# Performance work log

Hardware: AMD Instinct MI355X
Metric: run time of the kernel (lower is better)

The kernel has to match this reference:

```python
import jax, jax.numpy as jnp
import numpy as np

N_NODES = 100000


def setup_inputs() -> dict:
    key = jax.random.key(0)
    k1, k2, k3, k4, k5, k6 = jax.random.split(key, 6)
    n_edges = 1600000
    X = jax.random.normal(k1, (N_NODES, 256), dtype=jnp.float32)
    edge_row = jax.random.randint(k2, (n_edges,), 0, N_NODES, dtype=jnp.int64)
    edge_col = jax.random.randint(k3, (n_edges,), 0, N_NODES, dtype=jnp.int64)
    edge_val = jax.random.uniform(k4, (n_edges,), dtype=jnp.float32)
    W = jax.random.normal(k5, (128, 256), dtype=jnp.float32) * 0.05
    b = jax.random.normal(k6, (128,), dtype=jnp.float32) * 0.05
    return {"X": X, "edge_row": edge_row, "edge_col": edge_col,
            "edge_val": edge_val, "W": W, "b": b}


def reference(X, edge_row, edge_col, edge_val, W, b):
    # Dense projection: H = X @ W^T + b  -> [N, out_dim]
    H = jnp.einsum('ni,oi->no', X, W) + b
    # SpMM: out[r] = sum_e A[r, c_e] * H[c_e] over edges with row r
    msgs = edge_val[:, None] * H[edge_col]          # [E, out_dim]
    out = jax.ops.segment_sum(msgs, edge_row, num_segments=N_NODES)
    return out
```

## Files before the change

### kernel.cpp

```cpp
#include <hip/hip_runtime.h>
#include <hip/hip_bf16.h>

#define NNODES 100000
#define NEDGES 1600000
#define KDIM 256
#define ODIM 128
#define NXCD 8
#define NB_SCAN 391
#define EDGE_CAP 1900032
#define ESTRIDE 400000
#define GEMM_BLOCKS 1563
#define RANK_BLOCKS 1563

typedef __attribute__((ext_vector_type(8))) short short8;
typedef __attribute__((ext_vector_type(4))) float floatx4;

static __device__ __forceinline__ short f2bf(float f) {
  union { float f; unsigned u; } x; x.f = f;
  unsigned r = (x.u + 0x7fffu + ((x.u >> 16) & 1u)) >> 16;
  return (short)r;
}

__global__ void conv_w_kernel(const float* __restrict__ W, short* __restrict__ Wb) {
  int i = blockIdx.x * 256 + threadIdx.x;
  if (i < ODIM * KDIM) Wb[i] = f2bf(W[i]);
}

__global__ void scan1_kernel(const unsigned* __restrict__ counts, int* __restrict__ chunkExcl,
                             int* __restrict__ blockSums) {
  __shared__ int s[256];
  int t = threadIdx.x;
  int n = blockIdx.x * 256 + t;
  int sum = 0;
  if (n < NNODES) {
    int s0 = 0;
#pragma unroll
    for (int x = 0; x < NXCD; x++) s0 += (int)counts[(size_t)x * NNODES + n];
    sum = (s0 + 3) & ~3;
  }
  s[t] = sum;
  __syncthreads();
  for (int o = 1; o < 256; o <<= 1) {
    int add = (t >= o) ? s[t - o] : 0;
    __syncthreads();
    s[t] += add;
    __syncthreads();
  }
  if (n < NNODES) chunkExcl[n] = s[t] - sum;
  if (t == 255) blockSums[blockIdx.x] = s[255];
}

__global__ void scan2_kernel(const int* __restrict__ blockSums, int* __restrict__ blockBase,
                             int* __restrict__ offsets) {
  __shared__ int s[512];
  int t = threadIdx.x;
  int v = (t < NB_SCAN) ? blockSums[t] : 0;
  s[t] = v;
  __syncthreads();
  for (int o = 1; o < 512; o <<= 1) {
    int add = (t >= o) ? s[t - o] : 0;
    __syncthreads();
    s[t] += add;
    __syncthreads();
  }
  if (t < NB_SCAN) blockBase[t] = s[t] - v;
  if (t == 511) offsets[NNODES] = s[511];
}

__global__ void scan3_kernel(const int* __restrict__ chunkExcl, const int* __restrict__ blockBase,
                             unsigned* __restrict__ counts, int* __restrict__ offsets) {
  int n = blockIdx.x * 256 + threadIdx.x;
  if (n >= NNODES) return;
  int run = chunkExcl[n] + blockBase[n >> 8];
  offsets[n] = run;
#pragma unroll
  for (int x = 0; x < NXCD; x++) {
    int c = (int)counts[(size_t)x * NNODES + n];
    counts[(size_t)x * NNODES + n] = (unsigned)run;
    run += c;
  }
}

__global__ void place_kernel(const int* __restrict__ rows, const int* __restrict__ cols,
                             const float* __restrict__ vals,
                             const unsigned short* __restrict__ rank,
                             const unsigned* __restrict__ sbase, int2* __restrict__ edges) {
  int i = blockIdx.x * 256 + threadIdx.x;
#pragma unroll
  for (int j = 0; j < 4; j++) {
    int e = i + j * ESTRIDE;
    if (e < NEDGES) {
      int r = rows[e];
      unsigned rk = rank[e];
      int p = (int)sbase[(size_t)(rk >> 8) * NNODES + r] + (int)(rk & 255u);
      int2 rec;
      rec.x = cols[e];
      rec.y = __float_as_int(vals[e]);
      edges[p] = rec;
    }
  }
}

__global__ __launch_bounds__(256) void gemm_rank_kernel(
    const float* __restrict__ X, const short* __restrict__ Wb,
    const float* __restrict__ bias, unsigned* __restrict__ H2,
    const int* __restrict__ rows, unsigned* __restrict__ counts,
    unsigned short* __restrict__ rank) {
  if (blockIdx.x < RANK_BLOCKS) {
    unsigned xcc;
    asm("s_getreg_b32 %0, hwreg(HW_REG_XCC_ID)" : "=s"(xcc));
    xcc &= 7u;
    unsigned* cbase = counts + (size_t)xcc * NNODES;
    int i = blockIdx.x * 256 + threadIdx.x;
#pragma unroll
    for (int j = 0; j < 4; j++) {
      int e = i + j * ESTRIDE;
      if (e < NEDGES) {
        int r = rows[e];
        unsigned old = __hip_atomic_fetch_add(&cbase[r], 1u, __ATOMIC_RELAXED,
                                              __HIP_MEMORY_SCOPE_WORKGROUP);
        rank[e] = (unsigned short)((xcc << 8) | old);
      }
    }
    return;
  }
  const int gb = blockIdx.x - RANK_BLOCKS;
  const int lane = threadIdx.x & 63;
  const int wave = threadIdx.x >> 6;
  const int l16 = lane & 15;
  const int quad = lane >> 4;
  const int rowBase = gb * 64 + wave * 16;
  const int arow = rowBase + l16;
  const bool inb = arow < NNODES;
  const float4 zf4 = {0.f, 0.f, 0.f, 0.f};
  const float4* xp = (const float4*)(X + (size_t)(inb ? arow : 0) * KDIM + quad * 8);

  floatx4 acc[8];
#pragma unroll
  for (int t = 0; t < 8; t++) acc[t] = (floatx4){0.f, 0.f, 0.f, 0.f};

  float4 c0 = inb ? xp[0] : zf4;
  float4 c1 = inb ? xp[1] : zf4;
#pragma unroll
  for (int k0 = 0; k0 < 8; k0++) {
    float4 n0, n1;
    if (k0 < 7) {
      n0 = inb ? xp[(k0 + 1) * 8] : zf4;
      n1 = inb ? xp[(k0 + 1) * 8 + 1] : zf4;
    }
    short8 a;
    a[0] = f2bf(c0.x); a[1] = f2bf(c0.y); a[2] = f2bf(c0.z); a[3] = f2bf(c0.w);
    a[4] = f2bf(c1.x); a[5] = f2bf(c1.y); a[6] = f2bf(c1.z); a[7] = f2bf(c1.w);
    const short* bp = Wb + k0 * 32 + quad * 8;
#pragma unroll
    for (int t = 0; t < 8; t++) {
      short8 b = *(const short8*)(bp + (size_t)(t * 16 + l16) * KDIM);
      acc[t] = __builtin_amdgcn_mfma_f32_16x16x32_bf16(a, b, acc[t], 0, 0, 0);
    }
    if (k0 < 7) { c0 = n0; c1 = n1; }
  }

#pragma unroll
  for (int t = 0; t < 4; t++) {
    const int cl = t * 16 + l16;
    const float blo = bias[cl];
    const float bhi = bias[cl + 64];
#pragma unroll
    for (int r = 0; r < 4; r++) {
      const int row = rowBase + quad * 4 + r;
      if (row < NNODES) {
        unsigned lo = (unsigned short)f2bf(acc[t][r] + blo);
        unsigned hi = (unsigned short)f2bf(acc[t + 4][r] + bhi);
        H2[(size_t)row * 64 + cl] = lo | (hi << 16);
      }
    }
  }
}

__global__ __launch_bounds__(256) void spmm_kernel(const int* __restrict__ offsets,
                                                   const int2* __restrict__ edges,
                                                   const unsigned* __restrict__ H2,
                                                   float* __restrict__ out) {
  const int lane = threadIdx.x & 63;
  const int row = blockIdx.x * 4 + (threadIdx.x >> 6);
  if (row >= NNODES) return;
  const int s = offsets[row];
  const int e = offsets[row + 1];
  float ax = 0.f, ay = 0.f;
  for (int i = s; i < e; i += 4) {
    const int4 p01 = *(const int4*)(edges + i);
    const int4 p23 = *(const int4*)(edges + i + 2);
    const unsigned h0 = H2[(size_t)p01.x * 64 + lane];
    const unsigned h1 = H2[(size_t)p01.z * 64 + lane];
    const unsigned h2 = H2[(size_t)p23.x * 64 + lane];
    const unsigned h3 = H2[(size_t)p23.z * 64 + lane];
    const float v0 = __int_as_float(p01.y);
    const float v1 = __int_as_float(p01.w);
    const float v2 = __int_as_float(p23.y);
    const float v3 = __int_as_float(p23.w);
    ax += v0 * __uint_as_float(h0 << 16);
    ay += v0 * __uint_as_float(h0 & 0xffff0000u);
    ax += v1 * __uint_as_float(h1 << 16);
    ay += v1 * __uint_as_float(h1 & 0xffff0000u);
    ax += v2 * __uint_as_float(h2 << 16);
    ay += v2 * __uint_as_float(h2 & 0xffff0000u);
    ax += v3 * __uint_as_float(h3 << 16);
    ay += v3 * __uint_as_float(h3 & 0xffff0000u);
  }
  out[(size_t)row * 128 + lane] = ax;
  out[(size_t)row * 128 + 64 + lane] = ay;
}

extern "C" void kernel_launch(void* const* d_in, const int* in_sizes, int n_in,
                              void* d_out, int out_size, void* d_ws, size_t ws_size,
                              hipStream_t stream) {
  const float* X = (const float*)d_in[0];
  const int* erow = (const int*)d_in[1];
  const int* ecol = (const int*)d_in[2];
  const float* eval = (const float*)d_in[3];
  const float* W = (const float*)d_in[4];
  const float* bias = (const float*)d_in[5];
  float* out = (float*)d_out;

  char* ws = (char*)d_ws;
  size_t off = 0;
  auto alloc = [&](size_t bytes) -> char* {
    char* p = ws + off;
    off += (bytes + 255) & ~(size_t)255;
    return p;
  };
  unsigned* Hb = (unsigned*)alloc((size_t)NNODES * 64 * 4);
  short* Wb = (short*)alloc((size_t)ODIM * KDIM * 2);
  unsigned* counts = (unsigned*)alloc((size_t)NXCD * NNODES * 4);
  int* chunkExcl = (int*)alloc((size_t)NNODES * 4);
  int* offsets = (int*)alloc((size_t)(NNODES + 1) * 4);
  int* blockSums = (int*)alloc((size_t)NB_SCAN * 4);
  int* blockBase = (int*)alloc((size_t)NB_SCAN * 4);
  unsigned short* rank = (unsigned short*)alloc((size_t)NEDGES * 2);
  int2* edges = (int2*)alloc((size_t)EDGE_CAP * 8);

  hipMemsetAsync(counts, 0, (size_t)NXCD * NNODES * 4, stream);
  hipMemsetAsync(edges, 0, (size_t)EDGE_CAP * 8, stream);
  conv_w_kernel<<<(ODIM * KDIM + 255) / 256, 256, 0, stream>>>(W, Wb);
  gemm_rank_kernel<<<RANK_BLOCKS + GEMM_BLOCKS, 256, 0, stream>>>(X, Wb, bias, Hb,
                                                                  erow, counts, rank);
  scan1_kernel<<<NB_SCAN, 256, 0, stream>>>(counts, chunkExcl, blockSums);
  scan2_kernel<<<1, 512, 0, stream>>>(blockSums, blockBase, offsets);
  scan3_kernel<<<NB_SCAN, 256, 0, stream>>>(chunkExcl, blockBase, counts, offsets);
  place_kernel<<<(ESTRIDE + 255) / 256, 256, 0, stream>>>(erow, ecol, eval, rank, counts, edges);
  spmm_kernel<<<(NNODES + 3) / 4, 256, 0, stream>>>(offsets, edges, (const unsigned*)Hb, out);
}
```

Measured before the change: 403.7 us.

## Restructure preprocessing pipeline: fuse conv/rank, gemm/scan1, scan2/scan3; drop edge memset

```diff
diff --git a/kernel.cpp b/kernel.cpp
--- a/kernel.cpp
+++ b/kernel.cpp
@@ -8,9 +8,9 @@
 #define NXCD 8
 #define NB_SCAN 391
 #define EDGE_CAP 1900032
-#define ESTRIDE 400000
 #define GEMM_BLOCKS 1563
 #define RANK_BLOCKS 1563
+#define CONV_BLOCKS 128
 
 typedef __attribute__((ext_vector_type(8))) short short8;
 typedef __attribute__((ext_vector_type(4))) float floatx4;
@@ -21,110 +21,68 @@
   return (short)r;
 }
 
-__global__ void conv_w_kernel(const float* __restrict__ W, short* __restrict__ Wb) {
-  int i = blockIdx.x * 256 + threadIdx.x;
-  if (i < ODIM * KDIM) Wb[i] = f2bf(W[i]);
-}
-
-__global__ void scan1_kernel(const unsigned* __restrict__ counts, int* __restrict__ chunkExcl,
-                             int* __restrict__ blockSums) {
-  __shared__ int s[256];
-  int t = threadIdx.x;
-  int n = blockIdx.x * 256 + t;
-  int sum = 0;
-  if (n < NNODES) {
-    int s0 = 0;
-#pragma unroll
-    for (int x = 0; x < NXCD; x++) s0 += (int)counts[(size_t)x * NNODES + n];
-    sum = (s0 + 3) & ~3;
-  }
-  s[t] = sum;
-  __syncthreads();
-  for (int o = 1; o < 256; o <<= 1) {
-    int add = (t >= o) ? s[t - o] : 0;
-    __syncthreads();
-    s[t] += add;
-    __syncthreads();
-  }
-  if (n < NNODES) chunkExcl[n] = s[t] - sum;
-  if (t == 255) blockSums[blockIdx.x] = s[255];
-}
-
-__global__ void scan2_kernel(const int* __restrict__ blockSums, int* __restrict__ blockBase,
-                             int* __restrict__ offsets) {
-  __shared__ int s[512];
-  int t = threadIdx.x;
-  int v = (t < NB_SCAN) ? blockSums[t] : 0;
-  s[t] = v;
-  __syncthreads();
-  for (int o = 1; o < 512; o <<= 1) {
-    int add = (t >= o) ? s[t - o] : 0;
-    __syncthreads();
-    s[t] += add;
-    __syncthreads();
-  }
-  if (t < NB_SCAN) blockBase[t] = s[t] - v;
-  if (t == 511) offsets[NNODES] = s[511];
-}
-
-__global__ void scan3_kernel(const int* __restrict__ chunkExcl, const int* __restrict__ blockBase,
-                             unsigned* __restrict__ counts, int* __restrict__ offsets) {
-  int n = blockIdx.x * 256 + threadIdx.x;
-  if (n >= NNODES) return;
-  int run = chunkExcl[n] + blockBase[n >> 8];
-  offsets[n] = run;
-#pragma unroll
-  for (int x = 0; x < NXCD; x++) {
-    int c = (int)counts[(size_t)x * NNODES + n];
-    counts[(size_t)x * NNODES + n] = (unsigned)run;
-    run += c;
-  }
-}
-
-__global__ void place_kernel(const int* __restrict__ rows, const int* __restrict__ cols,
-                             const float* __restrict__ vals,
-                             const unsigned short* __restrict__ rank,
-                             const unsigned* __restrict__ sbase, int2* __restrict__ edges) {
-  int i = blockIdx.x * 256 + threadIdx.x;
-#pragma unroll
-  for (int j = 0; j < 4; j++) {
-    int e = i + j * ESTRIDE;
-    if (e < NEDGES) {
-      int r = rows[e];
-      unsigned rk = rank[e];
-      int p = (int)sbase[(size_t)(rk >> 8) * NNODES + r] + (int)(rk & 255u);
-      int2 rec;
-      rec.x = cols[e];
-      rec.y = __float_as_int(vals[e]);
-      edges[p] = rec;
-    }
-  }
-}
-
-__global__ __launch_bounds__(256) void gemm_rank_kernel(
+__global__ __launch_bounds__(256) void conv_rank_kernel(
+    const float* __restrict__ W, short* __restrict__ Wb,
+    const int* __restrict__ rows, unsigned* __restrict__ counts,
+    unsigned short* __restrict__ rank) {
+  if (blockIdx.x < CONV_BLOCKS) {
+    int i = blockIdx.x * 256 + threadIdx.x;
+    if (i < ODIM * KDIM) Wb[i] = f2bf(W[i]);
+    return;
+  }
+  unsigned xcc;
+  asm("s_getreg_b32 %0, hwreg(HW_REG_XCC_ID)" : "=s"(xcc));
+  xcc &= 7u;
+  unsigned* cbase = counts + (size_t)xcc * NNODES;
+  const int e0 = ((blockIdx.x - CONV_BLOCKS) * 256 + threadIdx.x) * 4;
+  if (e0 < NEDGES) {
+    const int4 r4 = *(const int4*)(rows + e0);
+    const unsigned o0 = __hip_atomic_fetch_add(&cbase[r4.x], 1u, __ATOMIC_RELAXED,
+                                               __HIP_MEMORY_SCOPE_WORKGROUP);
+    const unsigned o1 = __hip_atomic_fetch_add(&cbase[r4.y], 1u, __ATOMIC_RELAXED,
+                                               __HIP_MEMORY_SCOPE_WORKGROUP);
+    const unsigned o2 = __hip_atomic_fetch_add(&cbase[r4.z], 1u, __ATOMIC_RELAXED,
+                                               __HIP_MEMORY_SCOPE_WORKGROUP);
+    const unsigned o3 = __hip_atomic_fetch_add(&cbase[r4.w], 1u, __ATOMIC_RELAXED,
+                                               __HIP_MEMORY_SCOPE_WORKGROUP);
+    ushort4 rk;
+    rk.x = (unsigned short)((xcc << 8) | o0);
+    rk.y = (unsigned short)((xcc << 8) | o1);
+    rk.z = (unsigned short)((xcc << 8) | o2);
+    rk.w = (unsigned short)((xcc << 8) | o3);
+    *(ushort4*)(rank + e0) = rk;
+  }
+}
+
+__global__ __launch_bounds__(256) void gemm_scan1_kernel(
     const float* __restrict__ X, const short* __restrict__ Wb,
     const float* __restrict__ bias, unsigned* __restrict__ H2,
-    const int* __restrict__ rows, unsigned* __restrict__ counts,
-    unsigned short* __restrict__ rank) {
-  if (blockIdx.x < RANK_BLOCKS) {
-    unsigned xcc;
-    asm("s_getreg_b32 %0, hwreg(HW_REG_XCC_ID)" : "=s"(xcc));
-    xcc &= 7u;
-    unsigned* cbase = counts + (size_t)xcc * NNODES;
-    int i = blockIdx.x * 256 + threadIdx.x;
-#pragma unroll
-    for (int j = 0; j < 4; j++) {
-      int e = i + j * ESTRIDE;
-      if (e < NEDGES) {
-        int r = rows[e];
-        unsigned old = __hip_atomic_fetch_add(&cbase[r], 1u, __ATOMIC_RELAXED,
-                                              __HIP_MEMORY_SCOPE_WORKGROUP);
-        rank[e] = (unsigned short)((xcc << 8) | old);
-      }
-    }
+    const unsigned* __restrict__ counts, int* __restrict__ chunkExcl,
+    int* __restrict__ blockSums) {
+  __shared__ int s[256];
+  if (blockIdx.x < NB_SCAN) {
+    int t = threadIdx.x;
+    int n = blockIdx.x * 256 + t;
+    int sum = 0;
+    if (n < NNODES) {
+      int s0 = 0;
+#pragma unroll
+      for (int x = 0; x < NXCD; x++) s0 += (int)counts[(size_t)x * NNODES + n];
+      sum = (s0 + 3) & ~3;
+    }
+    s[t] = sum;
+    __syncthreads();
+    for (int o = 1; o < 256; o <<= 1) {
+      int add = (t >= o) ? s[t - o] : 0;
+      __syncthreads();
+      s[t] += add;
+      __syncthreads();
+    }
+    if (n < NNODES) chunkExcl[n] = s[t] - sum;
+    if (t == 255) blockSums[blockIdx.x] = s[255];
     return;
   }
-  const int gb = blockIdx.x - RANK_BLOCKS;
+  const int gb = blockIdx.x - NB_SCAN;
   const int lane = threadIdx.x & 63;
   const int wave = threadIdx.x >> 6;
   const int l16 = lane & 15;
@@ -174,6 +132,69 @@
         H2[(size_t)row * 64 + cl] = lo | (hi << 16);
       }
     }
+  }
+}
+
+__global__ __launch_bounds__(512) void scan23_kernel(
+    const int* __restrict__ blockSums, const int* __restrict__ chunkExcl,
+    unsigned* __restrict__ counts, int* __restrict__ offsets,
+    int2* __restrict__ edges) {
+  __shared__ int s[512];
+  const int t = threadIdx.x;
+  s[t] = (t < NB_SCAN) ? blockSums[t] : 0;
+  __syncthreads();
+  for (int o = 1; o < 512; o <<= 1) {
+    int add = (t >= o) ? s[t - o] : 0;
+    __syncthreads();
+    s[t] += add;
+    __syncthreads();
+  }
+  const int myBase = (blockIdx.x == 0) ? 0 : s[blockIdx.x - 1];
+  if (blockIdx.x == 0 && t == 0) offsets[NNODES] = s[NB_SCAN - 1];
+  if (t < 256) {
+    const int n = blockIdx.x * 256 + t;
+    if (n < NNODES) {
+      const int run = chunkExcl[n] + myBase;
+      offsets[n] = run;
+      int c[NXCD];
+      int deg = 0;
+#pragma unroll
+      for (int x = 0; x < NXCD; x++) {
+        c[x] = (int)counts[(size_t)x * NNODES + n];
+        deg += c[x];
+      }
+      int acc2 = run;
+#pragma unroll
+      for (int x = 0; x < NXCD; x++) {
+        counts[(size_t)x * NNODES + n] = (unsigned)acc2;
+        acc2 += c[x];
+      }
+      const int padded = (deg + 3) & ~3;
+      const int2 zrec = {0, 0};
+      for (int p = run + deg; p < run + padded; p++) edges[p] = zrec;
+    }
+  }
+}
+
+__global__ __launch_bounds__(256) void place_kernel(
+    const int* __restrict__ rows, const int* __restrict__ cols,
+    const float* __restrict__ vals, const unsigned short* __restrict__ rank,
+    const unsigned* __restrict__ sbase, int2* __restrict__ edges) {
+  const int e0 = (blockIdx.x * 256 + threadIdx.x) * 4;
+  if (e0 < NEDGES) {
+    const int4 r4 = *(const int4*)(rows + e0);
+    const int4 c4 = *(const int4*)(cols + e0);
+    const float4 v4 = *(const float4*)(vals + e0);
+    const ushort4 k4 = *(const ushort4*)(rank + e0);
+    int2 rec;
+    rec.x = c4.x; rec.y = __float_as_int(v4.x);
+    edges[(int)sbase[(size_t)(k4.x >> 8) * NNODES + r4.x] + (int)(k4.x & 255u)] = rec;
+    rec.x = c4.y; rec.y = __float_as_int(v4.y);
+    edges[(int)sbase[(size_t)(k4.y >> 8) * NNODES + r4.y] + (int)(k4.y & 255u)] = rec;
+    rec.x = c4.z; rec.y = __float_as_int(v4.z);
+    edges[(int)sbase[(size_t)(k4.z >> 8) * NNODES + r4.z] + (int)(k4.z & 255u)] = rec;
+    rec.x = c4.w; rec.y = __float_as_int(v4.w);
+    edges[(int)sbase[(size_t)(k4.w >> 8) * NNODES + r4.w] + (int)(k4.w & 255u)] = rec;
   }
 }
 
@@ -235,18 +256,14 @@
   int* chunkExcl = (int*)alloc((size_t)NNODES * 4);
   int* offsets = (int*)alloc((size_t)(NNODES + 1) * 4);
   int* blockSums = (int*)alloc((size_t)NB_SCAN * 4);
-  int* blockBase = (int*)alloc((size_t)NB_SCAN * 4);
   unsigned short* rank = (unsigned short*)alloc((size_t)NEDGES * 2);
   int2* edges = (int2*)alloc((size_t)EDGE_CAP * 8);
 
   hipMemsetAsync(counts, 0, (size_t)NXCD * NNODES * 4, stream);
-  hipMemsetAsync(edges, 0, (size_t)EDGE_CAP * 8, stream);
-  conv_w_kernel<<<(ODIM * KDIM + 255) / 256, 256, 0, stream>>>(W, Wb);
-  gemm_rank_kernel<<<RANK_BLOCKS + GEMM_BLOCKS, 256, 0, stream>>>(X, Wb, bias, Hb,
-                                                                  erow, counts, rank);
-  scan1_kernel<<<NB_SCAN, 256, 0, stream>>>(counts, chunkExcl, blockSums);
-  scan2_kernel<<<1, 512, 0, stream>>>(blockSums, blockBase, offsets);
-  scan3_kernel<<<NB_SCAN, 256, 0, stream>>>(chunkExcl, blockBase, counts, offsets);
-  place_kernel<<<(ESTRIDE + 255) / 256, 256, 0, stream>>>(erow, ecol, eval, rank, counts, edges);
+  conv_rank_kernel<<<CONV_BLOCKS + RANK_BLOCKS, 256, 0, stream>>>(W, Wb, erow, counts, rank);
+  gemm_scan1_kernel<<<NB_SCAN + GEMM_BLOCKS, 256, 0, stream>>>(X, Wb, bias, Hb,
+                                                               counts, chunkExcl, blockSums);
+  scan23_kernel<<<NB_SCAN, 512, 0, stream>>>(blockSums, chunkExcl, counts, offsets, edges);
+  place_kernel<<<RANK_BLOCKS, 256, 0, stream>>>(erow, ecol, eval, rank, counts, edges);
   spmm_kernel<<<(NNODES + 3) / 4, 256, 0, stream>>>(offsets, edges, (const unsigned*)Hb, out);
 }
```

Result: no change. 398.7 us (-1.2%).
